# Kernel optimization log

Hardware: AMD Instinct MI355X
Metric: run time of the kernel (lower is better)

The kernel has to match this reference:

```python
import jax, jax.numpy as jnp
import numpy as np
from jax.scipy.special import logsumexp
from jax.scipy.linalg import solve_triangular

STATE_DIM = 64
OBS_DIM = 32
NUM_PARTICLES = 32768
T = 64
DT = 0.01
DAMPING = 0.99
TEMPERATURE = 0.5
LOG_2PI = float(np.log(2.0 * np.pi))


def setup_inputs() -> dict:
    key = jax.random.key(0)
    ks = jax.random.split(key, 6)
    observations = jax.random.normal(ks[0], (T + 1, OBS_DIM), dtype=jnp.float32)
    A = 0.1 * jax.random.normal(ks[1], (STATE_DIM, STATE_DIM), dtype=jnp.float32)
    C = 0.1 * jax.random.normal(ks[2], (OBS_DIM, STATE_DIM), dtype=jnp.float32)
    Q_terms = 0.01 * jax.random.normal(ks[3], (STATE_DIM, STATE_DIM, STATE_DIM), dtype=jnp.float32)
    # torch init: eye * 0.1; add small perturbation so gradients are non-trivial
    Q_chol = 0.1 * jnp.eye(STATE_DIM, dtype=jnp.float32) + 0.005 * jax.random.normal(ks[4], (STATE_DIM, STATE_DIM), dtype=jnp.float32)
    R_chol = 0.1 * jnp.eye(OBS_DIM, dtype=jnp.float32) + 0.005 * jax.random.normal(ks[5], (OBS_DIM, OBS_DIM), dtype=jnp.float32)
    return {"observations": observations, "A": A, "C": C, "Q_terms": Q_terms,
            "Q_chol": Q_chol, "R_chol": R_chol}


def _obs_log_prob(particles, obs, C, L_R):
    """MVN log p(obs | C @ x, R) for each particle. particles [N,D], obs [obs_dim]."""
    mean = particles @ C.T                       # [N, obs_dim]
    diff = obs[None, :] - mean                   # [N, obs_dim]
    z = solve_triangular(L_R, diff.T, lower=True)  # [obs_dim, N]
    log_det_half = jnp.sum(jnp.log(jnp.diag(L_R)))
    return -0.5 * (OBS_DIM * LOG_2PI + jnp.sum(z * z, axis=0)) - log_det_half


def _smc_forward(observations, A, C, Q_terms, Q_chol, R_chol):
    R = R_chol @ R_chol.T
    L_R = jnp.linalg.cholesky(R)

    key = jax.random.key(42)
    k_init, k_scan = jax.random.split(key)
    particles = jax.random.normal(k_init, (NUM_PARTICLES, STATE_DIM), dtype=jnp.float32)
    log_weights = _obs_log_prob(particles, observations[0], C, L_R)

    def step(carry, xs):
        particles, log_weights, lml = carry
        obs_t, t = xs
        k = jax.random.fold_in(k_scan, t)
        k1, k2 = jax.random.split(k)

        log_w = log_weights - logsumexp(log_weights)
        u = jax.random.uniform(k1, (NUM_PARTICLES,), dtype=jnp.float32)
        gumbel = -jnp.log(-jnp.log(u + 1e-10) + 1e-10)
        ancestor_probs = jax.nn.softmax((log_w + gumbel) / TEMPERATURE)
        # Faithful to torch broadcast: collapses to the weighted-mean particle [1, D]
        resampled = (ancestor_probs @ particles)[None, :]

        noise = jax.random.normal(k2, (NUM_PARTICLES, STATE_DIM), dtype=jnp.float32) @ Q_chol.T
        quad = jnp.einsum('ijk,bj,bk->bi', Q_terms, resampled, resampled)  # [1, D]
        mean = resampled + DT * (resampled @ A.T + quad) * DAMPING          # [1, D]
        new_particles = mean + noise                                        # [N, D]

        new_log_weights = _obs_log_prob(new_particles, obs_t, C, L_R)
        new_lml = lml + logsumexp(new_log_weights)
        return (new_particles, new_log_weights, new_lml), None

    init = (particles, log_weights, jnp.zeros((), dtype=jnp.float32))
    (_, _, lml), _ = jax.lax.scan(step, init, (observations[1:], jnp.arange(T)))
    return lml[None]  # shape (1,) like torch


def reference(observations, A, C, Q_terms, Q_chol, R_chol):
    return _smc_forward(observations, A, C, Q_terms, Q_chol, R_chol)
```

## Files before the change

kernel.cpp:

```cpp
#include <hip/hip_runtime.h>
#include <cstdint>

#define NPART 32768
#define HALFN 16384

#define WS_W     0
#define WS_M     2048
#define WS_B     4096
#define WS_C0    6176
#define WS_KI    6178
#define WS_NK    6180
#define WS_UK    6308
#define WS_P4    6440
#define WS_PSE   8488
#define WS_QP64  24872
#define WS_END   25384

#define ATS32(p, v) __hip_atomic_store((p), (v), __ATOMIC_RELAXED, __HIP_MEMORY_SCOPE_AGENT)
#define ATL32(p)    __hip_atomic_load((p), __ATOMIC_RELAXED, __HIP_MEMORY_SCOPE_AGENT)
#define ATS64(p, v) __hip_atomic_store((p), (v), __ATOMIC_RELAXED, __HIP_MEMORY_SCOPE_AGENT)
#define ATL64(p)    __hip_atomic_load((p), __ATOMIC_RELAXED, __HIP_MEMORY_SCOPE_AGENT)

struct HK { uint32_t a, b; };

__host__ __device__ inline HK tf2x32(uint32_t k0, uint32_t k1, uint32_t x0, uint32_t x1) {
  uint32_t kx = k0 ^ k1 ^ 0x1BD11BDAu;
#define TF_R(r) { x0 += x1; x1 = (x1 << (r)) | (x1 >> (32 - (r))); x1 ^= x0; }
  x0 += k0; x1 += k1;
  TF_R(13) TF_R(15) TF_R(26) TF_R(6)
  x0 += k1; x1 += kx + 1u;
  TF_R(17) TF_R(29) TF_R(16) TF_R(24)
  x0 += kx; x1 += k0 + 2u;
  TF_R(13) TF_R(15) TF_R(26) TF_R(6)
  x0 += k0; x1 += k1 + 3u;
  TF_R(17) TF_R(29) TF_R(16) TF_R(24)
  x0 += k1; x1 += kx + 4u;
  TF_R(13) TF_R(15) TF_R(26) TF_R(6)
  x0 += kx; x1 += k0 + 5u;
#undef TF_R
  HK r; r.a = x0; r.b = x1; return r;
}

__device__ inline float erfinv_f(float x) {
  float w = -log1pf(-x * x);
  float p;
  if (w < 5.0f) {
    w -= 2.5f;
    p = 2.81022636e-08f;
    p = fmaf(p, w, 3.43273939e-07f);
    p = fmaf(p, w, -3.5233877e-06f);
    p = fmaf(p, w, -4.39150654e-06f);
    p = fmaf(p, w, 0.00021858087f);
    p = fmaf(p, w, -0.00125372503f);
    p = fmaf(p, w, -0.00417768164f);
    p = fmaf(p, w, 0.246640727f);
    p = fmaf(p, w, 1.50140941f);
  } else {
    w = sqrtf(w) - 3.0f;
    p = -0.000200214257f;
    p = fmaf(p, w, 0.000100950558f);
    p = fmaf(p, w, 0.00134934322f);
    p = fmaf(p, w, -0.00367342844f);
    p = fmaf(p, w, 0.00573950773f);
    p = fmaf(p, w, -0.0076224613f);
    p = fmaf(p, w, 0.00943887047f);
    p = fmaf(p, w, 1.00167406f);
    p = fmaf(p, w, 2.83297682f);
  }
  return p * x;
}

__device__ inline float u01(uint32_t bits) {
  return __uint_as_float((bits >> 9) | 0x3f800000u) - 1.0f;
}

__device__ inline uint64_t packfs(float v, uint32_t sq) {
  return ((uint64_t)sq << 32) | (uint64_t)__float_as_uint(v);
}

__global__ __launch_bounds__(1024) void kp_kernel(float* __restrict__ ws,
    const float* __restrict__ obs, const float* __restrict__ Cm,
    const float* __restrict__ Qc, const float* __restrict__ Rc) {
  __shared__ float Ls[32][32];
  __shared__ float Li[32][32];
  __shared__ float Wsh[32][64];
  const int tid = threadIdx.x;
  const int i = tid >> 5, j = tid & 31;
  uint32_t* wsu = (uint32_t*)ws;
  for (int idx = WS_P4 + tid; idx < WS_END; idx += 1024) wsu[idx] = 0u;
  if (tid <= 64) {
    HK p0 = tf2x32(0u, 42u, 0u, 2u);
    HK p1 = tf2x32(0u, 42u, 1u, 3u);
    uint32_t ks0 = p0.b, ks1 = p1.b;
    HK f = tf2x32(ks0, ks1, 0u, (uint32_t)tid);
    HK q0 = tf2x32(f.a, f.b, 0u, 2u);
    HK q1 = tf2x32(f.a, f.b, 1u, 3u);
    wsu[WS_UK + 2 * tid] = q0.a; wsu[WS_UK + 2 * tid + 1] = q1.a;
    if (tid < 64) { wsu[WS_NK + 2 * tid] = q0.b; wsu[WS_NK + 2 * tid + 1] = q1.b; }
    if (tid == 0) { wsu[WS_KI] = p0.a; wsu[WS_KI + 1] = p1.a; }
  }
  {
    float a = 0.0f;
    for (int k = 0; k < 32; ++k) a = fmaf(Rc[i * 32 + k], Rc[j * 32 + k], a);
    Ls[i][j] = a;
  }
  __syncthreads();
  for (int k = 0; k < 32; ++k) {
    if (tid == 0) Ls[k][k] = sqrtf(Ls[k][k]);
    __syncthreads();
    if (tid > k && tid < 32) Ls[tid][k] /= Ls[k][k];
    __syncthreads();
    if (i > k && j > k && j <= i) Ls[i][j] = fmaf(-Ls[i][k], Ls[j][k], Ls[i][j]);
    __syncthreads();
  }
  if (tid < 32) {
    for (int r = 0; r < 32; ++r) Li[r][tid] = 0.0f;
    Li[tid][tid] = 1.0f / Ls[tid][tid];
    for (int r = tid + 1; r < 32; ++r) {
      float s = 0.0f;
      for (int m = tid; m < r; ++m) s = fmaf(Ls[r][m], Li[m][tid], s);
      Li[r][tid] = -s / Ls[r][r];
    }
  }
  __syncthreads();
  if (tid == 0) {
    float ld = 0.0f;
    for (int k = 0; k < 32; ++k) ld += logf(Ls[k][k]);
    ws[WS_C0] = -0.5f * 32.0f * 1.8378770664093453f - ld;
  }
  for (int idx = tid; idx < 2048; idx += 1024) {
    int o = idx >> 6, d = idx & 63;
    float a = 0.0f;
    for (int k = 0; k < 32; ++k) a = fmaf(Li[o][k], Cm[k * 64 + d], a);
    Wsh[o][d] = a;
    ws[WS_W + idx] = a;
  }
  __syncthreads();
  for (int idx = tid; idx < 2048; idx += 1024) {
    int o = idx >> 6, d = idx & 63;
    float a = 0.0f;
    for (int k = 0; k < 64; ++k) a = fmaf(Wsh[o][k], Qc[k * 64 + d], a);
    ws[WS_M + idx] = a;
  }
  for (int idx = tid; idx < 2080; idx += 1024) {
    int t = idx >> 5, o = idx & 31;
    float a = 0.0f;
    for (int k = 0; k < 32; ++k) a = fmaf(Li[o][k], obs[t * 32 + k], a);
    ws[WS_B + idx] = a;
  }
}

__global__ __launch_bounds__(512, 2) void kmain_kernel(
    float* __restrict__ ws, const float* __restrict__ Am,
    const float* __restrict__ Qcg, const float* __restrict__ Qt,
    float* __restrict__ dout) {
  __shared__ __align__(16) float Ms[2048];
  __shared__ __align__(16) float Wm[2048];
  __shared__ __align__(16) float As[4096];
  __shared__ __align__(16) float Qcs[4096];
  __shared__ __align__(16) float Qs[1024];
  __shared__ float hC[32];
  __shared__ float rS[64], uS[64], mnS[64];
  __shared__ float ebL[256];
  __shared__ float redA[256], redB[256], redC[256], redD[256];
  __shared__ float SEw[8][64];
  __shared__ float wred[8][4];
  __shared__ float sc[8];
  __shared__ uint32_t keyL[260];

  const int tid = threadIdx.x;
  const int bid = blockIdx.x;
  uint32_t* wsu = (uint32_t*)ws;
  uint64_t* qp64 = (uint64_t*)(ws + WS_QP64);

  for (int i = tid; i < 2048; i += 512) { Ms[i] = ws[WS_M + i]; Wm[i] = ws[WS_W + i]; }
  for (int i = tid; i < 4096; i += 512) { As[i] = Am[i]; Qcs[i] = Qcg[i]; }
  {
    const int i0 = (bid >> 2) * 4096 + (bid & 3) * 1024;
    for (int i = tid; i < 1024; i += 512) Qs[i] = Qt[i0 + i];
  }
  for (int i = tid; i < 128; i += 512) keyL[i] = wsu[WS_NK + i];
  for (int i = tid; i < 130; i += 512) keyL[128 + i] = wsu[WS_UK + i];
  if (tid == 0) { keyL[258] = wsu[WS_KI]; keyL[259] = wsu[WS_KI + 1]; sc[4] = 0.0f; }
  if (tid < 32) hC[tid] = ws[WS_B + tid];
  const float C0 = ws[WS_C0];
  __syncthreads();

  const int pr = tid >> 3;
  const int l8 = tid & 7;
  const int p = bid * 64 + pr;
  const int d0 = l8 * 8;
  const int wv = tid >> 6, ln = tid & 63;

  float Elo[8], Ehi[8], gl, gh;
  float aL[4], aH[4];

  auto poll64 = [&](uint64_t* pp, uint32_t sq) -> float {
    uint64_t q;
    for (;;) {
      q = ATL64(pp);
      if ((uint32_t)(q >> 32) >= sq) break;
      __builtin_amdgcn_s_sleep(1);
    }
    return __uint_as_float((uint32_t)q);
  };

  auto genE8 = [&](uint32_t k0, uint32_t k1) {
    const uint32_t fb = (uint32_t)(p * 64 + d0);
#pragma unroll
    for (int j = 0; j < 8; ++j) {
      HK o = tf2x32(k0, k1, fb + (uint32_t)j, fb + (uint32_t)j + 1048576u);
      float fl = u01(o.a), fh = u01(o.b);
      float ul = fmaxf(-0.99999994f, fmaf(fl, 2.0f, -0.99999994f));
      float uh = fmaxf(-0.99999994f, fmaf(fh, 2.0f, -0.99999994f));
      Elo[j] = 1.41421354f * erfinv_f(ul);
      Ehi[j] = 1.41421354f * erfinv_f(uh);
    }
  };
  auto genG = [&](uint32_t k0, uint32_t k1) {
    HK og = tf2x32(k0, k1, (uint32_t)p, (uint32_t)(p + 16384));
    gl = -logf(-logf(u01(og.a) + 1e-10f) + 1e-10f);
    gh = -logf(-logf(u01(og.b) + 1e-10f) + 1e-10f);
  };

  auto ringME = [&](const float* matL) {
#pragma unroll
    for (int q = 0; q < 4; ++q) { aL[q] = 0.f; aH[q] = 0.f; }
#pragma unroll
    for (int k = 0; k < 8; ++k) {
      if (k) {
#pragma unroll
        for (int q = 0; q < 4; ++q) {
          aL[q] = __shfl(aL[q], (l8 + 1) & 7, 8);
          aH[q] = __shfl(aH[q], (l8 + 1) & 7, 8);
        }
      }
      const int ow = ((l8 + k) & 7) * 4;
#pragma unroll
      for (int q = 0; q < 4; ++q) {
        const float* mr = matL + (ow + q) * 64 + d0;
        float4 m0 = *(const float4*)mr;
        float4 m1 = *(const float4*)(mr + 4);
        float t0 = aL[q];
        t0 = fmaf(m0.x, Elo[0], t0); t0 = fmaf(m0.y, Elo[1], t0);
        t0 = fmaf(m0.z, Elo[2], t0); t0 = fmaf(m0.w, Elo[3], t0);
        t0 = fmaf(m1.x, Elo[4], t0); t0 = fmaf(m1.y, Elo[5], t0);
        t0 = fmaf(m1.z, Elo[6], t0); t0 = fmaf(m1.w, Elo[7], t0);
        aL[q] = t0;
        float t1 = aH[q];
        t1 = fmaf(m0.x, Ehi[0], t1); t1 = fmaf(m0.y, Ehi[1], t1);
        t1 = fmaf(m0.z, Ehi[2], t1); t1 = fmaf(m0.w, Ehi[3], t1);
        t1 = fmaf(m1.x, Ehi[4], t1); t1 = fmaf(m1.y, Ehi[5], t1);
        t1 = fmaf(m1.z, Ehi[6], t1); t1 = fmaf(m1.w, Ehi[7], t1);
        aH[q] = t1;
      }
    }
  };

  auto tailStore = [&](uint32_t sq) {
    const int ob = ((l8 + 7) & 7) * 4;
    float s2l = 0.f, s2h = 0.f;
#pragma unroll
    for (int q = 0; q < 4; ++q) {
      float zl = hC[ob + q] - aL[q], zh = hC[ob + q] - aH[q];
      s2l = fmaf(zl, zl, s2l); s2h = fmaf(zh, zh, s2h);
    }
#pragma unroll
    for (int m = 1; m < 8; m <<= 1) { s2l += __shfl_xor(s2l, m, 8); s2h += __shfl_xor(s2h, m, 8); }
    const float lwL = C0 - 0.5f * s2l, lwH = C0 - 0.5f * s2h;
    const float yl = (lwL + gl) * 2.0f, yh = (lwH + gh) * 2.0f;
    float mv = fmaxf(yl, yh), ml = fmaxf(lwL, lwH);
#pragma unroll
    for (int m = 1; m < 64; m <<= 1) {
      mv = fmaxf(mv, __shfl_xor(mv, m, 64));
      ml = fmaxf(ml, __shfl_xor(ml, m, 64));
    }
    if (ln == 0) { wred[wv][0] = mv; wred[wv][1] = ml; }
    __syncthreads();
    if (tid == 0) {
      float a = wred[0][0], b = wred[0][1];
      for (int q = 1; q < 8; ++q) { a = fmaxf(a, wred[q][0]); b = fmaxf(b, wred[q][1]); }
      sc[0] = a; sc[1] = b;
    }
    __syncthreads();
    const float myb = sc[0], mlb = sc[1];
    const float wLo = expf(yl - myb), wHi = expf(yh - myb);
    float vzy = (l8 == 0) ? (wLo + wHi) : 0.0f;
    float vzl = (l8 == 0) ? (expf(lwL - mlb) + expf(lwH - mlb)) : 0.0f;
#pragma unroll
    for (int m = 1; m < 64; m <<= 1) { vzy += __shfl_xor(vzy, m, 64); vzl += __shfl_xor(vzl, m, 64); }
    if (ln == 0) { wred[wv][2] = vzy; wred[wv][3] = vzl; }
    float v[8];
#pragma unroll
    for (int j = 0; j < 8; ++j) v[j] = fmaf(wHi, Ehi[j], wLo * Elo[j]);
#pragma unroll
    for (int m = 8; m < 64; m <<= 1) {
#pragma unroll
      for (int j = 0; j < 8; ++j) v[j] += __shfl_xor(v[j], m, 64);
    }
    if (ln < 8) {
#pragma unroll
      for (int j = 0; j < 8; ++j) SEw[wv][ln * 8 + j] = v[j];
    }
    __syncthreads();
    float zl2 = 0.0f;
    if (tid < 64) {
      float ssum = SEw[0][tid];
      for (int q = 1; q < 8; ++q) ssum += SEw[q][tid];
      ATS32(ws + WS_PSE + (bid << 6) + tid, ssum);
    }
    if (tid == 0) {
      float zy = wred[0][2];
      zl2 = wred[0][3];
      for (int q = 1; q < 8; ++q) { zy += wred[q][2]; zl2 += wred[q][3]; }
      float* pb = ws + WS_P4 + (bid << 3);
      ATS32(pb + 0, sc[0]);
      ATS32(pb + 1, sc[1]);
      ATS32(pb + 2, zy);
    }
    if (tid < 64) asm volatile("s_waitcnt vmcnt(0)" ::: "memory");
    if (tid == 0)
      ATS64((uint64_t*)(ws + WS_P4 + (bid << 3) + 4), packfs(zl2, sq));
  };

  auto combine = [&](int s) {
    const uint32_t sq = (uint32_t)(s + 1);
    if (tid < 256) {
      float* pb = ws + WS_P4 + (tid << 3);
      float zl = poll64((uint64_t*)(pb + 4), sq);
      asm volatile("" ::: "memory");
      redA[tid] = ATL32(pb + 0);
      redB[tid] = ATL32(pb + 1);
      redC[tid] = ATL32(pb + 2);
      redD[tid] = zl;
    }
    __syncthreads();
    float pse[32];
    const int d = tid & 63, c = tid >> 6;
#pragma unroll
    for (int b8 = 0; b8 < 32; ++b8)
      pse[b8] = ATL32(ws + WS_PSE + (((c << 5) + b8) << 6) + d);
    if (tid < 64) {
      const int l = tid;
      float a0 = redA[l], a1 = redA[l + 64], a2 = redA[l + 128], a3 = redA[l + 192];
      float b0 = redB[l], b1 = redB[l + 64], b2 = redB[l + 128], b3 = redB[l + 192];
      float myg = fmaxf(fmaxf(a0, a2), fmaxf(a1, a3));
      float mlg = fmaxf(fmaxf(b0, b2), fmaxf(b1, b3));
#pragma unroll
      for (int m = 32; m >= 1; m >>= 1) {
        myg = fmaxf(myg, __shfl_xor(myg, m, 64));
        mlg = fmaxf(mlg, __shfl_xor(mlg, m, 64));
      }
      myg = __shfl(myg, 0, 64); mlg = __shfl(mlg, 0, 64);
      float zy0 = redC[l], zy1 = redC[l + 64], zy2 = redC[l + 128], zy3 = redC[l + 192];
      float zl0 = redD[l], zl1 = redD[l + 64], zl2 = redD[l + 128], zl3 = redD[l + 192];
      float e0 = expf(a0 - myg), e1 = expf(a1 - myg), e2 = expf(a2 - myg), e3 = expf(a3 - myg);
      ebL[l] = e0; ebL[l + 64] = e1; ebL[l + 128] = e2; ebL[l + 192] = e3;
      float zyS = (e0 * zy0 + e2 * zy2) + (e1 * zy1 + e3 * zy3);
      float f0 = expf(b0 - mlg) * zl0, f1 = expf(b1 - mlg) * zl1;
      float f2 = expf(b2 - mlg) * zl2, f3 = expf(b3 - mlg) * zl3;
      float zlS = (f0 + f2) + (f1 + f3);
#pragma unroll
      for (int m = 32; m >= 1; m >>= 1) {
        zyS += __shfl_xor(zyS, m, 64);
        zlS += __shfl_xor(zlS, m, 64);
      }
      if (l == 0) {
        sc[2] = zyS;
        if (s > 0) sc[4] += mlg + logf(zlS);
      }
    }
    __syncthreads();
    const float Zy = sc[2];
    {
      float pp = 0.0f;
#pragma unroll
      for (int b8 = 0; b8 < 32; ++b8)
        pp = fmaf(ebL[(c << 5) + b8], pse[b8], pp);
      SEw[c][d] = pp;
    }
    __syncthreads();
    if (tid < 64) {
      float sg = SEw[0][tid];
      for (int cc = 1; cc < 8; ++cc) sg += SEw[cc][tid];
      uS[tid] = sg / Zy;
    }
    __syncthreads();
    if (tid < 64) {
      float r;
      if (s == 0) r = uS[tid];
      else {
        r = mnS[tid];
        const float* qr = Qcs + tid * 64;
        for (int k2 = 0; k2 < 64; ++k2) r = fmaf(uS[k2], qr[k2], r);
      }
      rS[tid] = r;
    }
    __syncthreads();
  };

  auto quadPub = [&](int s) {
    const uint32_t sq = (uint32_t)(s + 1);
    if (tid < 256) {
      const int jl = tid >> 4, kc = tid & 15;
      const float* qr = Qs + jl * 64 + kc * 4;
      float t0 = qr[0] * rS[kc * 4];
      t0 = fmaf(qr[1], rS[kc * 4 + 1], t0);
      t0 = fmaf(qr[2], rS[kc * 4 + 2], t0);
      t0 = fmaf(qr[3], rS[kc * 4 + 3], t0);
      redA[tid] = t0 * rS[(bid & 3) * 16 + jl];
    }
    __syncthreads();
    if (tid < 64) {
      float q0 = redA[tid], q1 = redA[tid + 64], q2 = redA[tid + 128], q3 = redA[tid + 192];
      float qs = (q0 + q2) + (q1 + q3);
#pragma unroll
      for (int m = 32; m >= 1; m >>= 1) qs += __shfl_xor(qs, m, 64);
      if (tid == 0) ATS64(qp64 + bid, packfs(qs, sq));
    }
  };

  auto meanH = [&](int s) {
    const uint32_t sq = (uint32_t)(s + 1);
    if (tid < 64) {
      float ar = 0.0f;
      const float* arow = As + tid * 64;
      for (int k2 = 0; k2 < 64; ++k2) ar = fmaf(arow[k2], rS[k2], ar);
      uint64_t* qb = qp64 + (tid << 2);
      uint64_t u0, u1, u2, u3;
      for (;;) {
        u0 = ATL64(qb + 0); u1 = ATL64(qb + 1);
        u2 = ATL64(qb + 2); u3 = ATL64(qb + 3);
        bool ok = ((uint32_t)(u0 >> 32) >= sq) && ((uint32_t)(u1 >> 32) >= sq) &&
                  ((uint32_t)(u2 >> 32) >= sq) && ((uint32_t)(u3 >> 32) >= sq);
        if (__all(ok)) break;
        __builtin_amdgcn_s_sleep(1);
      }
      float qd = __uint_as_float((uint32_t)u0) + __uint_as_float((uint32_t)u1) +
                 __uint_as_float((uint32_t)u2) + __uint_as_float((uint32_t)u3);
      mnS[tid] = rS[tid] + 0.0099f * (ar + qd);
    }
    __syncthreads();
    asm volatile("" ::: "memory");
    if (tid < 32) {
      float hv = ws[WS_B + (s + 1) * 32 + tid];
      const float* wrow = Wm + tid * 64;
      for (int d2 = 0; d2 < 64; ++d2) hv = fmaf(-wrow[d2], mnS[d2], hv);
      hC[tid] = hv;
    }
    __syncthreads();
  };

  genE8(keyL[258], keyL[259]);
  genG(keyL[128], keyL[129]);
  ringME(Wm);
  tailStore(1u);
  genE8(keyL[0], keyL[1]);

  for (int s = 0; s < 64; ++s) {
    combine(s);
    quadPub(s);
    genG(keyL[128 + 2 * (s + 1)], keyL[128 + 2 * (s + 1) + 1]);
    ringME(Ms);
    meanH(s);
    tailStore((uint32_t)(s + 2));
    if (s < 63)
      genE8(keyL[2 * (s + 1)], keyL[2 * (s + 1) + 1]);
  }

  if (bid == 0) {
    const uint32_t sq = 65u;
    float pml = 0.f, pzlv = 0.f;
    if (tid < 256) {
      float* pb = ws + WS_P4 + (tid << 3);
      pzlv = poll64((uint64_t*)(pb + 4), sq);
      asm volatile("" ::: "memory");
      pml = ATL32(pb + 1);
      redB[tid] = pml;
    }
    __syncthreads();
    for (int st = 128; st > 0; st >>= 1) {
      if (tid < st) redB[tid] = fmaxf(redB[tid], redB[tid + st]);
      __syncthreads();
    }
    const float mlwg = redB[0];
    __syncthreads();
    if (tid < 256) redB[tid] = expf(pml - mlwg) * pzlv;
    __syncthreads();
    for (int st = 128; st > 0; st >>= 1) {
      if (tid < st) redB[tid] += redB[tid + st];
      __syncthreads();
    }
    if (tid == 0) dout[0] = sc[4] + mlwg + logf(redB[0]);
  }
}

extern "C" void kernel_launch(void* const* d_in, const int* in_sizes, int n_in,
                              void* d_out, int out_size, void* d_ws, size_t ws_size,
                              hipStream_t stream) {
  const float* obs = (const float*)d_in[0];
  const float* Am = (const float*)d_in[1];
  const float* Cm = (const float*)d_in[2];
  const float* Qt = (const float*)d_in[3];
  const float* Qc = (const float*)d_in[4];
  const float* Rc = (const float*)d_in[5];
  float* ws = (float*)d_ws;
  float* out = (float*)d_out;
  (void)in_sizes; (void)n_in; (void)out_size; (void)ws_size;

  kp_kernel<<<dim3(1), dim3(1024), 0, stream>>>(ws, obs, Cm, Qc, Rc);

  void* params[] = { (void*)&ws, (void*)&Am, (void*)&Qc, (void*)&Qt, (void*)&out };
  hipLaunchCooperativeKernel((const void*)kmain_kernel, dim3(256), dim3(512),
                             params, 0, stream);
}
```

Baseline: 1.230 ms.

## Compute quadratic term per full row on 64 blocks and drop poll sleeps

The quadratic term Q_terms·r·r is now computed by only the first 64 blocks, each taking a full 64x64 row slab of Q, so one published partial per output dimension replaces four quarter partials. meanH now polls a single published value instead of four, and the spin loops in combine and meanH no longer sleep between polls. This is meant to cut the number of cross-block flags each step has to wait on and the polling latency, in exchange for more quadPub work per block on a subset of blocks, more shared memory, and heavier memory traffic from tight spinning.

```diff
diff --git a/kernel.cpp b/kernel.cpp
--- a/kernel.cpp
+++ b/kernel.cpp
@@ -158,7 +158,7 @@
   __shared__ __align__(16) float Wm[2048];
   __shared__ __align__(16) float As[4096];
   __shared__ __align__(16) float Qcs[4096];
-  __shared__ __align__(16) float Qs[1024];
+  __shared__ __align__(16) float Qrow[4096];
   __shared__ float hC[32];
   __shared__ float rS[64], uS[64], mnS[64];
   __shared__ float ebL[256];
@@ -175,9 +175,8 @@
 
   for (int i = tid; i < 2048; i += 512) { Ms[i] = ws[WS_M + i]; Wm[i] = ws[WS_W + i]; }
   for (int i = tid; i < 4096; i += 512) { As[i] = Am[i]; Qcs[i] = Qcg[i]; }
-  {
-    const int i0 = (bid >> 2) * 4096 + (bid & 3) * 1024;
-    for (int i = tid; i < 1024; i += 512) Qs[i] = Qt[i0 + i];
+  if (bid < 64) {
+    for (int i = tid; i < 4096; i += 512) Qrow[i] = Qt[bid * 4096 + i];
   }
   for (int i = tid; i < 128; i += 512) keyL[i] = wsu[WS_NK + i];
   for (int i = tid; i < 130; i += 512) keyL[128 + i] = wsu[WS_UK + i];
@@ -327,12 +326,16 @@
     const uint32_t sq = (uint32_t)(s + 1);
     if (tid < 256) {
       float* pb = ws + WS_P4 + (tid << 3);
-      float zl = poll64((uint64_t*)(pb + 4), sq);
+      uint64_t q;
+      for (;;) {
+        q = ATL64((uint64_t*)(pb + 4));
+        if ((uint32_t)(q >> 32) >= sq) break;
+      }
       asm volatile("" ::: "memory");
       redA[tid] = ATL32(pb + 0);
       redB[tid] = ATL32(pb + 1);
       redC[tid] = ATL32(pb + 2);
-      redD[tid] = zl;
+      redD[tid] = __uint_as_float((uint32_t)q);
     }
     __syncthreads();
     float pse[32];
@@ -403,20 +406,44 @@
     const uint32_t sq = (uint32_t)(s + 1);
     if (tid < 256) {
       const int jl = tid >> 4, kc = tid & 15;
-      const float* qr = Qs + jl * 64 + kc * 4;
-      float t0 = qr[0] * rS[kc * 4];
-      t0 = fmaf(qr[1], rS[kc * 4 + 1], t0);
-      t0 = fmaf(qr[2], rS[kc * 4 + 2], t0);
-      t0 = fmaf(qr[3], rS[kc * 4 + 3], t0);
-      redA[tid] = t0 * rS[(bid & 3) * 16 + jl];
+#pragma unroll
+      for (int q4 = 0; q4 < 4; ++q4) {
+        const float* qr = Qrow + (q4 * 16 + jl) * 64 + kc * 4;
+        float t0 = qr[0] * rS[kc * 4];
+        t0 = fmaf(qr[1], rS[kc * 4 + 1], t0);
+        t0 = fmaf(qr[2], rS[kc * 4 + 2], t0);
+        t0 = fmaf(qr[3], rS[kc * 4 + 3], t0);
+        t0 = t0 * rS[q4 * 16 + jl];
+        if (q4 == 0) redA[tid] = t0;
+        else if (q4 == 1) redB[tid] = t0;
+        else if (q4 == 2) redC[tid] = t0;
+        else redD[tid] = t0;
+      }
     }
     __syncthreads();
     if (tid < 64) {
-      float q0 = redA[tid], q1 = redA[tid + 64], q2 = redA[tid + 128], q3 = redA[tid + 192];
-      float qs = (q0 + q2) + (q1 + q3);
-#pragma unroll
-      for (int m = 32; m >= 1; m >>= 1) qs += __shfl_xor(qs, m, 64);
-      if (tid == 0) ATS64(qp64 + bid, packfs(qs, sq));
+      float pA, pB, pC, pD;
+      {
+        float q0 = redA[tid], q1 = redA[tid + 64], q2 = redA[tid + 128], q3 = redA[tid + 192];
+        pA = (q0 + q2) + (q1 + q3);
+        q0 = redB[tid]; q1 = redB[tid + 64]; q2 = redB[tid + 128]; q3 = redB[tid + 192];
+        pB = (q0 + q2) + (q1 + q3);
+        q0 = redC[tid]; q1 = redC[tid + 64]; q2 = redC[tid + 128]; q3 = redC[tid + 192];
+        pC = (q0 + q2) + (q1 + q3);
+        q0 = redD[tid]; q1 = redD[tid + 64]; q2 = redD[tid + 128]; q3 = redD[tid + 192];
+        pD = (q0 + q2) + (q1 + q3);
+      }
+#pragma unroll
+      for (int m = 32; m >= 1; m >>= 1) {
+        pA += __shfl_xor(pA, m, 64);
+        pB += __shfl_xor(pB, m, 64);
+        pC += __shfl_xor(pC, m, 64);
+        pD += __shfl_xor(pD, m, 64);
+      }
+      if (tid == 0) {
+        float qd = pA + pB + pC + pD;
+        ATS64(qp64 + bid, packfs(qd, sq));
+      }
     }
   };
 
@@ -426,18 +453,13 @@
       float ar = 0.0f;
       const float* arow = As + tid * 64;
       for (int k2 = 0; k2 < 64; ++k2) ar = fmaf(arow[k2], rS[k2], ar);
-      uint64_t* qb = qp64 + (tid << 2);
-      uint64_t u0, u1, u2, u3;
+      uint64_t u0;
+      uint64_t* qb = qp64 + tid;
       for (;;) {
-        u0 = ATL64(qb + 0); u1 = ATL64(qb + 1);
-        u2 = ATL64(qb + 2); u3 = ATL64(qb + 3);
-        bool ok = ((uint32_t)(u0 >> 32) >= sq) && ((uint32_t)(u1 >> 32) >= sq) &&
-                  ((uint32_t)(u2 >> 32) >= sq) && ((uint32_t)(u3 >> 32) >= sq);
-        if (__all(ok)) break;
-        __builtin_amdgcn_s_sleep(1);
-      }
-      float qd = __uint_as_float((uint32_t)u0) + __uint_as_float((uint32_t)u1) +
-                 __uint_as_float((uint32_t)u2) + __uint_as_float((uint32_t)u3);
+        u0 = ATL64(qb);
+        if ((uint32_t)(u0 >> 32) >= sq) break;
+      }
+      float qd = __uint_as_float((uint32_t)u0);
       mnS[tid] = rS[tid] + 0.0099f * (ar + qd);
     }
     __syncthreads();
@@ -459,7 +481,7 @@
 
   for (int s = 0; s < 64; ++s) {
     combine(s);
-    quadPub(s);
+    if (bid < 64) quadPub(s);
     genG(keyL[128 + 2 * (s + 1)], keyL[128 + 2 * (s + 1) + 1]);
     ringME(Ms);
     meanH(s);
```

Measured after the change: 1.348 ms. 9.5% more time.
